# Kernel tuning notes

Measured on AMD Instinct MI355X. Metric: run time of the kernel, lower is better.

Reference implementation:

```python
import jax, jax.numpy as jnp
import numpy as np

B, T, S, D = 8, 2048, 2048, 256


def setup_inputs() -> dict:
    key = jax.random.key(0)
    k1, k2, k3, k4 = jax.random.split(key, 4)
    source = jax.random.normal(k1, (B, T, D), dtype=jnp.float32)
    memory_bank = jax.random.normal(k2, (B, S, D), dtype=jnp.float32)
    # torch Linear(2*dim, dim, bias=False); stored as [in, out] so y = x @ W_out
    W_out = jax.random.normal(k3, (2 * D, D), dtype=jnp.float32) * 0.05
    memory_lengths = jax.random.randint(k4, (B,), 1, S + 1, dtype=jnp.int64)
    return {"source": source, "memory_bank": memory_bank, "W_out": W_out,
            "memory_lengths": memory_lengths}


def reference(source, memory_bank, W_out, memory_lengths):
    # align[b,t,s] = <source[b,t], memory_bank[b,s]>   (attn_type='dot')
    align = jnp.einsum('btd,bsd->bts', source, memory_bank)
    # sequence mask over source positions
    mask = jnp.arange(S)[None, :] < memory_lengths[:, None]          # [B,S]
    align = jnp.where(mask[:, None, :], align, -jnp.inf)             # [B,T,S]
    # coverage branch (multi-step): exp of shifted scores
    maxes = jnp.max(align, axis=2, keepdims=True)
    exp_score = jnp.exp(align - maxes)                               # [B,T,S]
    # tril-ones bmm == shifted cumulative sum over target steps:
    # penalty[t] = sum_{j<t} exp_score[j] for t>=1, penalty[0] = 1
    penalty = jnp.cumsum(exp_score[:, :-1, :], axis=1)
    penalty = jnp.concatenate(
        [jnp.ones_like(exp_score[:, :1, :]), penalty], axis=1)
    unnormalized = exp_score / (penalty + 1e-20)
    align_vectors = unnormalized / jnp.sum(unnormalized, axis=2, keepdims=True)
    # context and output projection
    c = jnp.einsum('bts,bsd->btd', align_vectors, memory_bank)
    concat_c = jnp.concatenate([c, source], axis=-1)                 # [B,T,2D]
    attn_h = jnp.tanh(concat_c @ W_out)                              # [B,T,D]
    return attn_h, align_vectors
```

## Files before the change

### kernel.cpp

```cpp
#include <hip/hip_runtime.h>
#include <math.h>

#define BN 8
#define TT 2048
#define SS 2048
#define DD 256
#define NSEG 128
#define SEGLEN 16

typedef __attribute__((ext_vector_type(8))) short short8;
typedef __attribute__((ext_vector_type(4))) float floatx4;

__device__ __forceinline__ unsigned short f2bf_rne(float f) {
    unsigned int u = __float_as_uint(f);
    u = (u + 0x7FFFu + ((u >> 16) & 1u)) >> 16;
    return (unsigned short)u;
}
__device__ __forceinline__ float bf2f(unsigned short h) {
    return __uint_as_float(((unsigned int)h) << 16);
}
__device__ __forceinline__ unsigned int fenc(float f) {
    unsigned int b = __float_as_uint(f);
    return (b & 0x80000000u) ? ~b : (b | 0x80000000u);
}
__device__ __forceinline__ float fdec(unsigned int u) {
    return __uint_as_float((u & 0x80000000u) ? (u & 0x7FFFFFFFu) : ~u);
}

__device__ __forceinline__ void async16(const unsigned short* g, unsigned short* l) {
    __builtin_amdgcn_global_load_lds(
        (const __attribute__((address_space(1))) unsigned int*)g,
        (__attribute__((address_space(3))) unsigned int*)l,
        16, 0, 0);
}

__global__ __launch_bounds__(256) void kprep(
    const float* __restrict__ src, const float* __restrict__ mem,
    unsigned short* __restrict__ shi, unsigned short* __restrict__ slo,
    unsigned short* __restrict__ mhirm, unsigned short* __restrict__ mlorm,
    unsigned short* __restrict__ mhi, unsigned int* __restrict__ rowmaxU)
{
    if (blockIdx.y == 2) {
        const int gid = blockIdx.x * 256 + threadIdx.x;
        const int lane = gid & 63;
        const int dt   = (gid >> 6) & 15;
        const int c    = (gid >> 10) & 63;
        const int b    = gid >> 16;
        const int quad = lane >> 4, n = lane & 15;
        const int s = c * 32 + quad * 8;
        const int d = dt * 16 + n;
        const float* srcp = mem + ((size_t)b * SS + s) * DD + d;
        short8 hi;
#pragma unroll
        for (int j = 0; j < 8; j++)
            hi[j] = (short)f2bf_rne(srcp[(size_t)j * DD]);
        *(short8*)(mhi + (size_t)gid * 8) = hi;
        return;
    }
    if (blockIdx.y == 0 && blockIdx.x < (BN * TT / 256))
        rowmaxU[blockIdx.x * 256 + threadIdx.x] = 0u;
    const float* in; unsigned short *oh, *ol;
    if (blockIdx.y == 0) { in = src; oh = shi; ol = slo; }
    else                 { in = mem; oh = mhirm; ol = mlorm; }
    const size_t base = ((size_t)blockIdx.x * 256 + threadIdx.x) * 8;
    float4 v0 = *(const float4*)(in + base);
    float4 v1 = *(const float4*)(in + base + 4);
    float f[8] = {v0.x, v0.y, v0.z, v0.w, v1.x, v1.y, v1.z, v1.w};
    short8 hv, lv;
#pragma unroll
    for (int j = 0; j < 8; j++) {
        unsigned short h = f2bf_rne(f[j]);
        hv[j] = (short)h;
        lv[j] = (short)f2bf_rne(f[j] - bf2f(h));
    }
    *(short8*)(oh + base) = hv;
    *(short8*)(ol + base) = lv;
}

__global__ __launch_bounds__(256) void k1_mfma(
    const unsigned short* __restrict__ shi, const unsigned short* __restrict__ slo,
    const unsigned short* __restrict__ mhirm, const unsigned short* __restrict__ mlorm,
    const int* __restrict__ lens, float* __restrict__ alignb,
    unsigned int* __restrict__ rowmaxU)
{
    const int b  = blockIdx.z;
    const int len = lens[b];
    const int s0 = blockIdx.x * 128;
    if (s0 >= len) return;
    const int t0 = blockIdx.y * 128;
    const int tid = threadIdx.x;
    const int wave = tid >> 6, lane = tid & 63;
    const int wt = wave & 1, wsb = wave >> 1;
    const int quad = lane >> 4, m = lane & 15;

    __shared__ unsigned short ldsAh[128 * 32];
    __shared__ unsigned short ldsAl[128 * 32];
    __shared__ unsigned short ldsBh[128 * 32];
    __shared__ unsigned short ldsBl[128 * 32];

    const int srow = tid >> 2, sk4 = (tid & 3) * 8;
    const size_t aBase = ((size_t)(b * TT + t0 + srow)) * DD + sk4;
    const size_t bBase = ((size_t)(b * SS + s0 + srow)) * DD + sk4;
    const size_t aBase2 = aBase + (size_t)64 * DD;
    const size_t bBase2 = bBase + (size_t)64 * DD;
    const int lo1 = tid * 8, lo2 = tid * 8 + 2048;

    floatx4 acc[4][4];
#pragma unroll
    for (int i = 0; i < 4; i++)
#pragma unroll
        for (int j = 0; j < 4; j++) acc[i][j] = (floatx4)0.f;

    for (int kc = 0; kc < 8; kc++) {
        const int ko = kc * 32;
        __syncthreads();
        async16(shi   + aBase  + ko, ldsAh + lo1);
        async16(shi   + aBase2 + ko, ldsAh + lo2);
        async16(slo   + aBase  + ko, ldsAl + lo1);
        async16(slo   + aBase2 + ko, ldsAl + lo2);
        async16(mhirm + bBase  + ko, ldsBh + lo1);
        async16(mhirm + bBase2 + ko, ldsBh + lo2);
        async16(mlorm + bBase  + ko, ldsBl + lo1);
        async16(mlorm + bBase2 + ko, ldsBl + lo2);
        __syncthreads();

        short8 Ah[4], Al[4], Bh[4], Bl[4];
#pragma unroll
        for (int f = 0; f < 4; f++) {
            const int ra = (wt * 64 + f * 16 + m) * 32 + quad * 8;
            const int rb = (wsb * 64 + f * 16 + m) * 32 + quad * 8;
            Ah[f] = *(const short8*)&ldsAh[ra];
            Al[f] = *(const short8*)&ldsAl[ra];
            Bh[f] = *(const short8*)&ldsBh[rb];
            Bl[f] = *(const short8*)&ldsBl[rb];
        }
#pragma unroll
        for (int mf = 0; mf < 4; mf++)
#pragma unroll
            for (int nf = 0; nf < 4; nf++) {
                acc[mf][nf] = __builtin_amdgcn_mfma_f32_16x16x32_bf16(
                    Ah[mf], Bh[nf], acc[mf][nf], 0, 0, 0);
                acc[mf][nf] = __builtin_amdgcn_mfma_f32_16x16x32_bf16(
                    Al[mf], Bh[nf], acc[mf][nf], 0, 0, 0);
                acc[mf][nf] = __builtin_amdgcn_mfma_f32_16x16x32_bf16(
                    Ah[mf], Bl[nf], acc[mf][nf], 0, 0, 0);
            }
    }

#pragma unroll
    for (int mf = 0; mf < 4; mf++)
#pragma unroll
        for (int reg = 0; reg < 4; reg++) {
            const int t = t0 + wt * 64 + mf * 16 + quad * 4 + reg;
            float* row = alignb + ((size_t)(b * TT + t)) * SS + s0 + wsb * 64 + m;
#pragma unroll
            for (int nf = 0; nf < 4; nf++)
                row[nf * 16] = acc[mf][nf][reg];
        }

    if (s0 + wsb * 64 < len) {
#pragma unroll
        for (int mf = 0; mf < 4; mf++)
#pragma unroll
            for (int reg = 0; reg < 4; reg++) {
                float mx = -INFINITY;
#pragma unroll
                for (int nf = 0; nf < 4; nf++) {
                    const int col = s0 + wsb * 64 + nf * 16 + m;
                    mx = (col < len) ? fmaxf(mx, acc[mf][nf][reg]) : mx;
                }
#pragma unroll
                for (int off = 1; off < 16; off <<= 1)
                    mx = fmaxf(mx, __shfl_xor(mx, off, 64));
                if (m == 0) {
                    const int t = t0 + wt * 64 + mf * 16 + quad * 4 + reg;
                    atomicMax(&rowmaxU[b * TT + t], fenc(mx));
                }
            }
    }
}

__global__ __launch_bounds__(256) void k3_segsum(
    const float* __restrict__ alignb, const unsigned int* __restrict__ rowmaxU,
    const int* __restrict__ lens, float* __restrict__ segsum)
{
    const int b = blockIdx.z, seg = blockIdx.y;
    const int s4 = (blockIdx.x * 256 + threadIdx.x) * 4;
    const int len = lens[b];
    float4 sum = {0.f, 0.f, 0.f, 0.f};
    if (s4 < len) {
        const float* base = alignb + ((size_t)b * TT + seg * SEGLEN) * SS + s4;
        const unsigned int* rmu = rowmaxU + b * TT + seg * SEGLEN;
        const bool v1 = (s4 + 1) < len, v2 = (s4 + 2) < len, v3 = (s4 + 3) < len;
#pragma unroll 4
        for (int r = 0; r < SEGLEN; r++) {
            const float m = fdec(rmu[r]);
            float4 v = *(const float4*)(base + (size_t)r * SS);
            sum.x += __expf(v.x - m);
            sum.y += v1 ? __expf(v.y - m) : 0.f;
            sum.z += v2 ? __expf(v.z - m) : 0.f;
            sum.w += v3 ? __expf(v.w - m) : 0.f;
        }
    }
    *(float4*)(segsum + ((size_t)b * NSEG + seg) * SS + s4) = sum;
}

__global__ __launch_bounds__(256) void k4_prefix(float* __restrict__ segsum)
{
    const int b = blockIdx.y;
    const int s = blockIdx.x * 256 + threadIdx.x;
    float run = 0.f;
    for (int g = 0; g < NSEG / 8; g++) {
        float v[8];
#pragma unroll
        for (int i = 0; i < 8; i++)
            v[i] = segsum[((size_t)b * NSEG + g * 8 + i) * SS + s];
#pragma unroll
        for (int i = 0; i < 8; i++) {
            segsum[((size_t)b * NSEG + g * 8 + i) * SS + s] = run;
            run += v[i];
        }
    }
}

__global__ __launch_bounds__(256) void k5_scan(
    float* __restrict__ alignb, const unsigned int* __restrict__ rowmaxU,
    const float* __restrict__ segsum, const int* __restrict__ lens)
{
    const int seg = blockIdx.x, b = blockIdx.y;
    const int len = lens[b];
    const int c0 = threadIdx.x * 8;
    const int lane = threadIdx.x & 63, wid = threadIdx.x >> 6;
    const bool anyv = c0 < len;

    __shared__ float red[8];

    float psum[8];
    {
        const float* sp = segsum + ((size_t)b * NSEG + seg) * SS + c0;
        float4 a = *(const float4*)sp, c = *(const float4*)(sp + 4);
        psum[0] = a.x; psum[1] = a.y; psum[2] = a.z; psum[3] = a.w;
        psum[4] = c.x; psum[5] = c.y; psum[6] = c.z; psum[7] = c.w;
    }

    float* rowp = alignb + ((size_t)(b * TT + seg * SEGLEN)) * SS + c0;

    float avn[8] = {0.f, 0.f, 0.f, 0.f, 0.f, 0.f, 0.f, 0.f};
    if (anyv) {
        float4 a = *(const float4*)rowp, c = *(const float4*)(rowp + 4);
        avn[0] = a.x; avn[1] = a.y; avn[2] = a.z; avn[3] = a.w;
        avn[4] = c.x; avn[5] = c.y; avn[6] = c.z; avn[7] = c.w;
    }

    for (int r = 0; r < SEGLEN; r++) {
        const int t = seg * SEGLEN + r;
        const float m = fdec(rowmaxU[b * TT + t]);
        float av[8];
#pragma unroll
        for (int j = 0; j < 8; j++) av[j] = avn[j];
        if (anyv && r + 1 < SEGLEN) {
            const float* np = rowp + (size_t)(r + 1) * SS;
            float4 a = *(const float4*)np, c = *(const float4*)(np + 4);
            avn[0] = a.x; avn[1] = a.y; avn[2] = a.z; avn[3] = a.w;
            avn[4] = c.x; avn[5] = c.y; avn[6] = c.z; avn[7] = c.w;
        }
        float u[8], rsum = 0.f;
#pragma unroll
        for (int j = 0; j < 8; j++) {
            float e = (c0 + j < len) ? __expf(av[j] - m) : 0.f;
            float div = (t == 0) ? 1.0f : (psum[j] + 1e-20f);
            u[j] = e * __builtin_amdgcn_rcpf(div);
            psum[j] += e;
            rsum += u[j];
        }
#pragma unroll
        for (int off = 32; off > 0; off >>= 1)
            rsum += __shfl_down(rsum, off, 64);
        const int pp = (r & 1) * 4;
        if (lane == 0) red[pp + wid] = rsum;
        __syncthreads();
        const float inv = 1.0f / (red[pp] + red[pp + 1] + red[pp + 2] + red[pp + 3]);
        float* wp = rowp + (size_t)r * SS;
        float4 o0 = {u[0] * inv, u[1] * inv, u[2] * inv, u[3] * inv};
        float4 o1 = {u[4] * inv, u[5] * inv, u[6] * inv, u[7] * inv};
        *(float4*)wp = o0;
        *(float4*)(wp + 4) = o1;
    }
}

__global__ __launch_bounds__(256) void k67_ctx_out(
    const float* __restrict__ alignb, const unsigned short* __restrict__ mhi,
    const int* __restrict__ lens, const float* __restrict__ src,
    const float* __restrict__ W, float* __restrict__ attn)
{
    const int b  = blockIdx.x;
    const int t0 = blockIdx.y * 32;
    const int tid  = threadIdx.x;
    const int wave = tid >> 6, lane = tid & 63;
    const int quad = lane >> 4, m = lane & 15;

    __shared__ __align__(16) float cT[32][256];
    __shared__ __align__(16) float wT[32][256];
    __shared__ float xT[32][32];

    const int len = lens[b];
    int cmax = (len + 31) >> 5;
    if (cmax > 64) cmax = 64;

    floatx4 acc[2][4];
#pragma unroll
    for (int i = 0; i < 2; i++)
#pragma unroll
        for (int j = 0; j < 4; j++) acc[i][j] = (floatx4)0.f;

    const float* aBase = alignb + ((size_t)(b * TT + t0 + m)) * SS + quad * 8;

    for (int c = 0; c < cmax; c++) {
        short8 Bf[4];
#pragma unroll
        for (int j = 0; j < 4; j++) {
            const int dt = wave * 4 + j;
            Bf[j] = *(const short8*)(mhi +
                (((size_t)(b * 64 + c) * 16 + dt) * 64 + lane) * 8);
        }
#pragma unroll
        for (int mf = 0; mf < 2; mf++) {
            const float* ap = aBase + (size_t)(mf * 16) * SS + c * 32;
            float4 v0 = *(const float4*)ap;
            float4 v1 = *(const float4*)(ap + 4);
            union { short8 s; unsigned int u[4]; } pk;
            pk.u[0] = (__float_as_uint(v0.x) >> 16) | (__float_as_uint(v0.y) & 0xFFFF0000u);
            pk.u[1] = (__float_as_uint(v0.z) >> 16) | (__float_as_uint(v0.w) & 0xFFFF0000u);
            pk.u[2] = (__float_as_uint(v1.x) >> 16) | (__float_as_uint(v1.y) & 0xFFFF0000u);
            pk.u[3] = (__float_as_uint(v1.z) >> 16) | (__float_as_uint(v1.w) & 0xFFFF0000u);
#pragma unroll
            for (int j = 0; j < 4; j++)
                acc[mf][j] = __builtin_amdgcn_mfma_f32_16x16x32_bf16(
                    pk.s, Bf[j], acc[mf][j], 0, 0, 0);
        }
    }

#pragma unroll
    for (int mf = 0; mf < 2; mf++)
#pragma unroll
        for (int j = 0; j < 4; j++) {
            const int d = wave * 64 + j * 16 + m;
#pragma unroll
            for (int reg = 0; reg < 4; reg++)
                cT[mf * 16 + quad * 4 + reg][d] = acc[mf][j][reg];
        }

    const int tx = tid & 63, ty = tid >> 6;

    float4 oacc[8];
#pragma unroll
    for (int i = 0; i < 8; i++) oacc[i] = make_float4(0.f, 0.f, 0.f, 0.f);

    for (int k0 = 0; k0 < 2 * DD; k0 += 32) {
        __syncthreads();
#pragma unroll
        for (int it = 0; it < 8; it++) {
            int f = tid + it * 256;
            int kr = f >> 6, col = (f & 63) * 4;
            *(float4*)&wT[kr][col] =
                *(const float4*)(W + (size_t)(k0 + kr) * DD + col);
        }
#pragma unroll
        for (int rep = 0; rep < 4; rep++) {
            int idx = tid + rep * 256;
            int r = idx >> 5, c = idx & 31;
            int k = k0 + c;
            float x;
            if (k < DD) {
                x = cT[r][k];
            } else {
                x = src[((size_t)b * TT + t0 + r) * DD + (k - DD)];
            }
            xT[r][c] = x;
        }
        __syncthreads();
#pragma unroll
        for (int kk = 0; kk < 32; kk++) {
            float4 w4 = *(const float4*)&wT[kk][tx * 4];
#pragma unroll
            for (int r4 = 0; r4 < 8; r4++) {
                float x = xT[ty + r4 * 4][kk];
                oacc[r4].x += x * w4.x; oacc[r4].y += x * w4.y;
                oacc[r4].z += x * w4.z; oacc[r4].w += x * w4.w;
            }
        }
    }
#pragma unroll
    for (int r4 = 0; r4 < 8; r4++) {
        const int t = t0 + ty + r4 * 4;
        float4 o;
        o.x = tanhf(oacc[r4].x); o.y = tanhf(oacc[r4].y);
        o.z = tanhf(oacc[r4].z); o.w = tanhf(oacc[r4].w);
        *(float4*)(attn + ((size_t)b * TT + t) * DD + tx * 4) = o;
    }
}

extern "C" void kernel_launch(void* const* d_in, const int* in_sizes, int n_in,
                              void* d_out, int out_size, void* d_ws, size_t ws_size,
                              hipStream_t stream)
{
    const float* src  = (const float*)d_in[0];
    const float* mem  = (const float*)d_in[1];
    const float* Wout = (const float*)d_in[2];
    const int*   lens = (const int*)d_in[3];

    float* out    = (float*)d_out;
    float* attn   = out;
    float* alignb = out + (size_t)BN * TT * DD;

    unsigned int* rowmaxU = (unsigned int*)d_ws;
    float* segsum = (float*)(rowmaxU + (size_t)BN * TT);
    unsigned short* mhi = (unsigned short*)(segsum + (size_t)BN * NSEG * SS);
    unsigned short* shi   = mhi + (size_t)BN * SS * DD;
    unsigned short* slo   = shi + (size_t)BN * TT * DD;
    unsigned short* mhirm = slo + (size_t)BN * TT * DD;
    unsigned short* mlorm = mhirm + (size_t)BN * SS * DD;

    kprep<<<dim3(BN * TT * DD / (256 * 8), 3), 256, 0, stream>>>(
        src, mem, shi, slo, mhirm, mlorm, mhi, rowmaxU);
    k1_mfma<<<dim3(SS / 128, TT / 128, BN), 256, 0, stream>>>(
        shi, slo, mhirm, mlorm, lens, alignb, rowmaxU);
    k3_segsum<<<dim3(SS / 1024, NSEG, BN), 256, 0, stream>>>(alignb, rowmaxU, lens, segsum);
    k4_prefix<<<dim3(SS / 256, BN), 256, 0, stream>>>(segsum);
    k5_scan<<<dim3(NSEG, BN), 256, 0, stream>>>(alignb, rowmaxU, segsum, lens);
    k67_ctx_out<<<dim3(BN, TT / 32), 256, 0, stream>>>(
        alignb, mhi, lens, src, Wout, attn);
}
```

Measured before the change: 437.6 us.

## Split context and output projection into separate kernels with LDS-staged align tiles

```diff
diff --git a/kernel.cpp b/kernel.cpp
--- a/kernel.cpp
+++ b/kernel.cpp
@@ -288,46 +288,57 @@
     }
 }
 
-__global__ __launch_bounds__(256) void k67_ctx_out(
+__global__ __launch_bounds__(256, 4) void k6_context(
     const float* __restrict__ alignb, const unsigned short* __restrict__ mhi,
-    const int* __restrict__ lens, const float* __restrict__ src,
-    const float* __restrict__ W, float* __restrict__ attn)
+    const int* __restrict__ lens, float* __restrict__ cfull)
 {
     const int b  = blockIdx.x;
-    const int t0 = blockIdx.y * 32;
+    const int t0 = blockIdx.y * 16;
     const int tid  = threadIdx.x;
     const int wave = tid >> 6, lane = tid & 63;
     const int quad = lane >> 4, m = lane & 15;
 
-    __shared__ __align__(16) float cT[32][256];
-    __shared__ __align__(16) float wT[32][256];
-    __shared__ float xT[32][32];
-
     const int len = lens[b];
-    int cmax = (len + 31) >> 5;
-    if (cmax > 64) cmax = 64;
-
-    floatx4 acc[2][4];
-#pragma unroll
-    for (int i = 0; i < 2; i++)
-#pragma unroll
-        for (int j = 0; j < 4; j++) acc[i][j] = (floatx4)0.f;
-
-    const float* aBase = alignb + ((size_t)(b * TT + t0 + m)) * SS + quad * 8;
-
-    for (int c = 0; c < cmax; c++) {
-        short8 Bf[4];
-#pragma unroll
-        for (int j = 0; j < 4; j++) {
-            const int dt = wave * 4 + j;
-            Bf[j] = *(const short8*)(mhi +
-                (((size_t)(b * 64 + c) * 16 + dt) * 64 + lane) * 8);
-        }
-#pragma unroll
-        for (int mf = 0; mf < 2; mf++) {
-            const float* ap = aBase + (size_t)(mf * 16) * SS + c * 32;
-            float4 v0 = *(const float4*)ap;
-            float4 v1 = *(const float4*)(ap + 4);
+    int nch = (len + 127) >> 7;
+    if (nch > 16) nch = 16;
+
+    __shared__ __align__(16) unsigned char ldsA[16 * 512];
+
+    floatx4 acc[4];
+#pragma unroll
+    for (int j = 0; j < 4; j++) acc[j] = (floatx4)0.f;
+
+    const char* aRow0 = (const char*)(alignb + ((size_t)(b * TT + t0)) * SS);
+
+    const int flat0 = tid * 16;
+    const int flat1 = 4096 + tid * 16;
+    const int row0 = flat0 >> 9, row1 = flat1 >> 9;
+    const int col0 = (flat0 ^ ((row0 & 7) << 4)) & 511;
+    const int col1 = (flat1 ^ ((row1 & 7) << 4)) & 511;
+    const char* src0 = aRow0 + (size_t)row0 * (SS * 4) + col0;
+    const char* src1 = aRow0 + (size_t)row1 * (SS * 4) + col1;
+
+    for (int cc = 0; cc < nch; cc++) {
+        __syncthreads();
+        async16((const unsigned short*)(src0 + cc * 512),
+                (unsigned short*)(ldsA + flat0));
+        async16((const unsigned short*)(src1 + cc * 512),
+                (unsigned short*)(ldsA + flat1));
+        __syncthreads();
+
+#pragma unroll
+        for (int c4 = 0; c4 < 4; c4++) {
+            const int c = cc * 4 + c4;
+            short8 Bf[4];
+#pragma unroll
+            for (int j = 0; j < 4; j++) {
+                const int dt = wave * 4 + j;
+                Bf[j] = *(const short8*)(mhi +
+                    (((size_t)(b * 64 + c) * 16 + dt) * 64 + lane) * 8);
+            }
+            const int lb = (m * 512 + c4 * 128 + quad * 32) ^ ((m & 7) << 4);
+            float4 v0 = *(const float4*)(ldsA + lb);
+            float4 v1 = *(const float4*)(ldsA + (lb ^ 16));
             union { short8 s; unsigned int u[4]; } pk;
             pk.u[0] = (__float_as_uint(v0.x) >> 16) | (__float_as_uint(v0.y) & 0xFFFF0000u);
             pk.u[1] = (__float_as_uint(v0.z) >> 16) | (__float_as_uint(v0.w) & 0xFFFF0000u);
@@ -335,26 +346,37 @@
             pk.u[3] = (__float_as_uint(v1.z) >> 16) | (__float_as_uint(v1.w) & 0xFFFF0000u);
 #pragma unroll
             for (int j = 0; j < 4; j++)
-                acc[mf][j] = __builtin_amdgcn_mfma_f32_16x16x32_bf16(
-                    pk.s, Bf[j], acc[mf][j], 0, 0, 0);
-        }
-    }
-
-#pragma unroll
-    for (int mf = 0; mf < 2; mf++)
-#pragma unroll
-        for (int j = 0; j < 4; j++) {
-            const int d = wave * 64 + j * 16 + m;
-#pragma unroll
-            for (int reg = 0; reg < 4; reg++)
-                cT[mf * 16 + quad * 4 + reg][d] = acc[mf][j][reg];
-        }
-
+                acc[j] = __builtin_amdgcn_mfma_f32_16x16x32_bf16(
+                    pk.s, Bf[j], acc[j], 0, 0, 0);
+        }
+    }
+
+#pragma unroll
+    for (int j = 0; j < 4; j++) {
+        const int d = wave * 64 + j * 16 + m;
+#pragma unroll
+        for (int reg = 0; reg < 4; reg++) {
+            const int t = t0 + quad * 4 + reg;
+            cfull[((size_t)(b * TT + t)) * DD + d] = acc[j][reg];
+        }
+    }
+}
+
+__global__ __launch_bounds__(256) void k7_out(
+    const float* __restrict__ cfull, const float* __restrict__ src,
+    const float* __restrict__ W, float* __restrict__ attn)
+{
+    const int b = blockIdx.y;
+    const int t0 = blockIdx.x * 32;
+    const int tid = threadIdx.x;
     const int tx = tid & 63, ty = tid >> 6;
 
-    float4 oacc[8];
-#pragma unroll
-    for (int i = 0; i < 8; i++) oacc[i] = make_float4(0.f, 0.f, 0.f, 0.f);
+    __shared__ __align__(16) float wT[32][256];
+    __shared__ float xT[32][32];
+
+    float4 acc[8];
+#pragma unroll
+    for (int i = 0; i < 8; i++) acc[i] = make_float4(0.f, 0.f, 0.f, 0.f);
 
     for (int k0 = 0; k0 < 2 * DD; k0 += 32) {
         __syncthreads();
@@ -372,7 +394,7 @@
             int k = k0 + c;
             float x;
             if (k < DD) {
-                x = cT[r][k];
+                x = cfull[((size_t)b * TT + t0 + r) * DD + k];
             } else {
                 x = src[((size_t)b * TT + t0 + r) * DD + (k - DD)];
             }
@@ -385,8 +407,8 @@
 #pragma unroll
             for (int r4 = 0; r4 < 8; r4++) {
                 float x = xT[ty + r4 * 4][kk];
-                oacc[r4].x += x * w4.x; oacc[r4].y += x * w4.y;
-                oacc[r4].z += x * w4.z; oacc[r4].w += x * w4.w;
+                acc[r4].x += x * w4.x; acc[r4].y += x * w4.y;
+                acc[r4].z += x * w4.z; acc[r4].w += x * w4.w;
             }
         }
     }
@@ -394,8 +416,8 @@
     for (int r4 = 0; r4 < 8; r4++) {
         const int t = t0 + ty + r4 * 4;
         float4 o;
-        o.x = tanhf(oacc[r4].x); o.y = tanhf(oacc[r4].y);
-        o.z = tanhf(oacc[r4].z); o.w = tanhf(oacc[r4].w);
+        o.x = tanhf(acc[r4].x); o.y = tanhf(acc[r4].y);
+        o.z = tanhf(acc[r4].z); o.w = tanhf(acc[r4].w);
         *(float4*)(attn + ((size_t)b * TT + t) * DD + tx * 4) = o;
     }
 }
@@ -420,6 +442,7 @@
     unsigned short* slo   = shi + (size_t)BN * TT * DD;
     unsigned short* mhirm = slo + (size_t)BN * TT * DD;
     unsigned short* mlorm = mhirm + (size_t)BN * SS * DD;
+    float* cfull = (float*)shi;
 
     kprep<<<dim3(BN * TT * DD / (256 * 8), 3), 256, 0, stream>>>(
         src, mem, shi, slo, mhirm, mlorm, mhi, rowmaxU);
@@ -428,6 +451,6 @@
     k3_segsum<<<dim3(SS / 1024, NSEG, BN), 256, 0, stream>>>(alignb, rowmaxU, lens, segsum);
     k4_prefix<<<dim3(SS / 256, BN), 256, 0, stream>>>(segsum);
     k5_scan<<<dim3(NSEG, BN), 256, 0, stream>>>(alignb, rowmaxU, segsum, lens);
-    k67_ctx_out<<<dim3(BN, TT / 32), 256, 0, stream>>>(
-        alignb, mhi, lens, src, Wout, attn);
-}
+    k6_context<<<dim3(BN, TT / 16), 256, 0, stream>>>(alignb, mhi, lens, cfull);
+    k7_out<<<dim3(TT / 32, BN), 256, 0, stream>>>(cfull, src, Wout, attn);
+}
```

New measurement: 423.0 us. -3.3%, faster.
